# Performance work log

Hardware: AMD Instinct MI355X
Metric: run time of the kernel (lower is better)

The kernel has to match this reference:

```python
import jax, jax.numpy as jnp
import numpy as np

NUM_HEADS = 32
MAX_BIAS_LENGTH = 1024
ROPE_BASE = 10000.0


def _rope_cos_sin(seq_len, head_dim, dtype):
    half = head_dim // 2
    inv_freq = 1.0 / (ROPE_BASE ** (jnp.arange(0, half, dtype=jnp.float32) / half))
    t = jnp.arange(seq_len, dtype=jnp.float32)
    freqs = jnp.outer(t, inv_freq)  # [S, half]
    return jnp.cos(freqs).astype(dtype), jnp.sin(freqs).astype(dtype)


def _apply_rope(x, cos, sin):
    # x: [B, S, H, D]; non-interleaved (GPT-NeoX / flash-attn style) rotary
    half = x.shape[-1] // 2
    x1, x2 = x[..., :half], x[..., half:]
    c = cos[None, :, None, :]
    s = sin[None, :, None, :]
    return jnp.concatenate([x1 * c - x2 * s, x1 * s + x2 * c], axis=-1)


def setup_inputs() -> dict:
    key = jax.random.key(0)
    ks = jax.random.split(key, 7)
    B, S, Dm = 2, 2048, 2048
    std = 1.0 / np.sqrt(Dm)
    return {
        "hidden_states": jax.random.normal(ks[0], (B, S, Dm), jnp.float32),
        "Wq": jax.random.normal(ks[1], (Dm, Dm), jnp.float32) * std,
        "Wk": jax.random.normal(ks[2], (Dm, Dm), jnp.float32) * std,
        "Wv": jax.random.normal(ks[3], (Dm, Dm), jnp.float32) * std,
        "Wo": jax.random.normal(ks[4], (Dm, Dm), jnp.float32) * std,
        "learnable_bias": jax.random.normal(ks[5], (NUM_HEADS, MAX_BIAS_LENGTH), jnp.float32) * 0.001,
        "softmax_offset": jnp.zeros((NUM_HEADS,), jnp.float32),
    }


def reference(hidden_states, Wq, Wk, Wv, Wo, learnable_bias, softmax_offset):
    B, S, Dm = hidden_states.shape
    H = NUM_HEADS
    D = Dm // H
    scale = D ** -0.5

    # projections (nn.Linear: x @ W.T)
    q = (hidden_states @ Wq.T).reshape(B, S, H, D)
    k = (hidden_states @ Wk.T).reshape(B, S, H, D)
    v = (hidden_states @ Wv.T).reshape(B, S, H, D)

    cos, sin = _rope_cos_sin(S, D, q.dtype)
    q = _apply_rope(q, cos, sin)
    k = _apply_rope(k, cos, sin)

    q = q.transpose(0, 2, 1, 3)  # [B, H, S, D]
    k = k.transpose(0, 2, 1, 3)
    v = v.transpose(0, 2, 1, 3)

    scores = jnp.einsum("bhid,bhjd->bhij", q, k) * scale  # [B, H, S, S]

    # per-diagonal learnable bias: diag = i - j in [0, MAX_BIAS_LENGTH)
    i = jnp.arange(S)[:, None]
    j = jnp.arange(S)[None, :]
    diag = i - j  # [S, S]
    causal = diag >= 0
    in_band = causal & (diag < MAX_BIAS_LENGTH)
    bias = jnp.where(in_band, learnable_bias[:, jnp.clip(diag, 0, MAX_BIAS_LENGTH - 1)], 0.0)  # [H, S, S]
    scores = scores + bias[None]
    scores = jnp.where(causal[None, None], scores, -jnp.inf)

    # softmax with learnable per-head offset (attention-sink logit)
    off = softmax_offset[None, :, None]  # [1, H, 1]
    m = jnp.maximum(jnp.max(scores, axis=-1), off)  # [B, H, S]
    p = jnp.exp(scores - m[..., None])
    denom = jnp.sum(p, axis=-1) + jnp.exp(off - m)  # [B, H, S]
    out = jnp.einsum("bhij,bhjd->bhid", p, v) / denom[..., None]

    out = out.transpose(0, 2, 1, 3).reshape(B, S, Dm)
    return out @ Wo.T
```

## Files before the change

### kernel.cpp

```cpp
#include <hip/hip_runtime.h>
#include <hip/hip_bf16.h>
#include <stdint.h>

typedef __bf16 bf16x8 __attribute__((ext_vector_type(8)));
typedef float f32x4 __attribute__((ext_vector_type(4)));
typedef unsigned short u16;
typedef u16 u16x4 __attribute__((ext_vector_type(4)));

#define S_LEN 2048
#define DMODEL 2048
#define NHEADS 32
#define BATCH 2
#define MROWS (BATCH * S_LEN)
#define BIAS_LEN 1024

__device__ __forceinline__ u16 b16(float f) {
  union { __bf16 h; u16 u; } cv; cv.h = (__bf16)f; return cv.u;
}

__device__ __forceinline__ void gload16(const void* g, void* l) {
  __builtin_amdgcn_global_load_lds(
      (const __attribute__((address_space(1))) uint32_t*)g,
      (__attribute__((address_space(3))) uint32_t*)l, 16, 0, 0);
}

__global__ __launch_bounds__(256)
void cvt_bf16(const float* __restrict__ in, u16* __restrict__ out, int n) {
  int i = (blockIdx.x * 256 + threadIdx.x) * 4;
  if (i >= n) return;
  float4 v = *(const float4*)(in + i);
  u16x4 o = { b16(v.x), b16(v.y), b16(v.z), b16(v.w) };
  *(u16x4*)(out + i) = o;
}

__global__ __launch_bounds__(256)
void rope_tab(float* __restrict__ ct, float* __restrict__ st) {
  int idx = blockIdx.x * 256 + threadIdx.x;
  if (idx >= S_LEN * 32) return;
  int s = idx >> 5, d = idx & 31;
  float inv = exp2f((float)d * (-13.287712379549449f / 32.0f));
  float a = (float)s * inv;
  ct[idx] = cosf(a);
  st[idx] = sinf(a);
}

template<int EPI>
__global__ __launch_bounds__(256)
void gemm_bt(const u16* __restrict__ A, const u16* __restrict__ Bm,
             void* __restrict__ Cout,
             const float* __restrict__ ctab, const float* __restrict__ stab)
{
  __shared__ u16 sA[128 * 64];
  __shared__ u16 sB[128 * 64];
  const int tid  = threadIdx.x;
  const int lane = tid & 63;
  const int wid  = tid >> 6;
  const int wm   = wid >> 1, wn = wid & 1;
  const int lc   = lane & 15, lr = lane >> 4;
  const int tm   = blockIdx.y * 128;
  const int tn   = blockIdx.x * 128;

  f32x4 acc[4][4] = {};

  const u16* aS[4]; const u16* bS[4];
#pragma unroll
  for (int it = 0; it < 4; ++it) {
    int u = it * 256 + tid;
    int row = u >> 3;
    int ch  = (u & 7) ^ (row & 7);
    aS[it] = A  + (size_t)(tm + row) * DMODEL + ch * 8;
    bS[it] = Bm + (size_t)(tn + row) * DMODEL + ch * 8;
  }

  for (int k0 = 0; k0 < DMODEL; k0 += 64) {
    __syncthreads();
#pragma unroll
    for (int it = 0; it < 4; ++it) {
      int u = it * 256 + tid;
      gload16(aS[it] + k0, (char*)sA + u * 16);
      gload16(bS[it] + k0, (char*)sB + u * 16);
    }
    __syncthreads();
#pragma unroll
    for (int kk = 0; kk < 2; ++kk) {
      bf16x8 af[4], bq[4];
#pragma unroll
      for (int mi = 0; mi < 4; ++mi) {
        int row = wm * 64 + mi * 16 + lc;
        int ch  = (kk * 4 + lr) ^ (row & 7);
        af[mi] = *(const bf16x8*)((const char*)sA + row * 128 + ch * 16);
      }
#pragma unroll
      for (int ni = 0; ni < 4; ++ni) {
        int row = wn * 64 + ni * 16 + lc;
        int ch  = (kk * 4 + lr) ^ (row & 7);
        bq[ni] = *(const bf16x8*)((const char*)sB + row * 128 + ch * 16);
      }
#pragma unroll
      for (int mi = 0; mi < 4; ++mi)
#pragma unroll
        for (int ni = 0; ni < 4; ++ni)
          acc[mi][ni] = __builtin_amdgcn_mfma_f32_16x16x32_bf16(af[mi], bq[ni], acc[mi][ni], 0, 0, 0);
    }
  }

  if constexpr (EPI == 4) {
    float* C = (float*)Cout;
#pragma unroll
    for (int mi = 0; mi < 4; ++mi)
#pragma unroll
      for (int ni = 0; ni < 4; ++ni)
#pragma unroll
        for (int j = 0; j < 4; ++j) {
          int r = tm + wm * 64 + mi * 16 + lr * 4 + j;
          int c = tn + wn * 64 + ni * 16 + lc;
          C[(size_t)r * DMODEL + c] = acc[mi][ni][j];
        }
  } else if constexpr (EPI == 3) {
    u16* C = (u16*)Cout;
#pragma unroll
    for (int mi = 0; mi < 4; ++mi)
#pragma unroll
      for (int ni = 0; ni < 4; ++ni) {
        int col = tn + wn * 64 + ni * 16 + lc;
        int hh = col >> 6, d = col & 63;
        int m0 = tm + wm * 64 + mi * 16 + lr * 4;
        int bb = m0 >> 11, s = m0 & 2047;
        u16x4 v = { b16(acc[mi][ni][0]), b16(acc[mi][ni][1]),
                    b16(acc[mi][ni][2]), b16(acc[mi][ni][3]) };
        *(u16x4*)(C + (((size_t)bb * NHEADS + hh) * 64 + d) * S_LEN + s) = v;
      }
  } else {
    u16* C = (u16*)Cout;
#pragma unroll
    for (int mi = 0; mi < 4; ++mi)
#pragma unroll
      for (int ni = 0; ni < 2; ++ni)
#pragma unroll
        for (int j = 0; j < 4; ++j) {
          int col = tn + wn * 64 + ni * 16 + lc;
          int hh = col >> 6, dl = col & 63;
          int r = tm + wm * 64 + mi * 16 + lr * 4 + j;
          int bb = r >> 11, s = r & 2047;
          float x1 = acc[mi][ni][j], x2 = acc[mi][ni + 2][j];
          float cv = ctab[s * 32 + dl], sv = stab[s * 32 + dl];
          float o1 = x1 * cv - x2 * sv;
          float o2 = x1 * sv + x2 * cv;
          if constexpr (EPI == 1) { o1 *= 0.125f; o2 *= 0.125f; }
          size_t base = (((size_t)bb * NHEADS + hh) * S_LEN + s) * 64 + dl;
          C[base]      = b16(o1);
          C[base + 32] = b16(o2);
        }
  }
}

__global__ __launch_bounds__(512)
void attn_kernel(const u16* __restrict__ Q, const u16* __restrict__ K,
                 const u16* __restrict__ V, const float* __restrict__ biasg,
                 const float* __restrict__ offg, u16* __restrict__ O)
{
  __shared__ __align__(16) u16 sK[2][64 * 64];
  __shared__ __align__(16) u16 sV[2][64 * 64];
  __shared__ __align__(16) u16 sP[8][16 * 72];
  __shared__ float sBias[BIAS_LEN];

  const int tid = threadIdx.x, lane = tid & 63, wid = tid >> 6;
  const int lc = lane & 15, lr = lane >> 4;
  const int pi = blockIdx.x;
  const int bh = blockIdx.y;
  const int h  = bh & 31;
  const int b  = bh >> 5;
  const int qtA  = 31 - pi;
  const int myQt = (wid < 4) ? qtA : pi;
  const int qw   = myQt * 64 + (wid & 3) * 16;

  for (int i = tid; i < BIAS_LEN; i += 512) sBias[i] = biasg[h * BIAS_LEN + i];
  const float off = offg[h];

  const u16* qp = Q + ((size_t)bh * S_LEN + qw + lc) * 64;
  bf16x8 aq0 = *(const bf16x8*)(qp + lr * 8);
  bf16x8 aq1 = *(const bf16x8*)(qp + 32 + lr * 8);

  const int srow = tid >> 3;
  const int sch  = (tid & 7) ^ (srow & 7);
  const u16* kSrc = K + ((size_t)bh * S_LEN + srow) * 64 + sch * 8;
  const u16* vSrc = V + ((size_t)bh * 64 + srow) * S_LEN + sch * 8;

  float m = off, lsum = 1.0f;
  f32x4 o[4] = {};

  gload16(kSrc, (char*)sK[0] + tid * 16);
  gload16(vSrc, (char*)sV[0] + tid * 16);
  __syncthreads();

  for (int t = 0; t <= qtA; ++t) {
    const int cur = t & 1;
    if (t < qtA) {
      gload16(kSrc + (size_t)(t + 1) * 64 * 64, (char*)sK[cur ^ 1] + tid * 16);
      gload16(vSrc + (t + 1) * 64,              (char*)sV[cur ^ 1] + tid * 16);
    }

    if (t <= myQt) {
      const int kt = t * 64;
      f32x4 sc[4];
#pragma unroll
      for (int f = 0; f < 4; ++f) {
        int row = f * 16 + lc;
        bf16x8 k0 = *(const bf16x8*)((const char*)sK[cur] + row * 128 + ((lr) ^ (row & 7)) * 16);
        bf16x8 k1 = *(const bf16x8*)((const char*)sK[cur] + row * 128 + ((4 + lr) ^ (row & 7)) * 16);
        f32x4 z = {};
        z     = __builtin_amdgcn_mfma_f32_16x16x32_bf16(k0, aq0, z, 0, 0, 0);
        sc[f] = __builtin_amdgcn_mfma_f32_16x16x32_bf16(k1, aq1, z, 0, 0, 0);
      }

      const int db  = qw + lc - kt;
      const int dqt = qw - kt;
      float pvv[4][4];
      if (t == myQt) {
#pragma unroll
        for (int f = 0; f < 4; ++f)
#pragma unroll
          for (int j = 0; j < 4; ++j) {
            int dd = db - (f * 16 + lr * 4 + j);
            float bb = sBias[dd & 1023];
            pvv[f][j] = (dd >= 0) ? sc[f][j] + bb : -1e30f;
          }
      } else if (dqt <= 1008) {
#pragma unroll
        for (int f = 0; f < 4; ++f)
#pragma unroll
          for (int j = 0; j < 4; ++j)
            pvv[f][j] = sc[f][j] + sBias[db - (f * 16 + lr * 4 + j)];
      } else if (dqt < 1088) {
#pragma unroll
        for (int f = 0; f < 4; ++f)
#pragma unroll
          for (int j = 0; j < 4; ++j) {
            int dd = db - (f * 16 + lr * 4 + j);
            float bb = (dd < 1024) ? sBias[dd & 1023] : 0.0f;
            pvv[f][j] = sc[f][j] + bb;
          }
      } else {
#pragma unroll
        for (int f = 0; f < 4; ++f)
#pragma unroll
          for (int j = 0; j < 4; ++j)
            pvv[f][j] = sc[f][j];
      }

      float pmax = -1e30f;
#pragma unroll
      for (int f = 0; f < 4; ++f) {
        float a = fmaxf(fmaxf(pvv[f][0], pvv[f][1]), fmaxf(pvv[f][2], pvv[f][3]));
        pmax = fmaxf(pmax, a);
      }
      pmax = fmaxf(pmax, __shfl_xor(pmax, 16, 64));
      pmax = fmaxf(pmax, __shfl_xor(pmax, 32, 64));

      if (__any(pmax > m + 8.0f)) {
        float mn = fmaxf(m, pmax);
        float al = __expf(m - mn);
        m = mn;
        lsum *= al;
        float aj[4];
#pragma unroll
        for (int j = 0; j < 4; ++j) aj[j] = __shfl(al, lr * 4 + j, 64);
#pragma unroll
        for (int f2 = 0; f2 < 4; ++f2)
#pragma unroll
          for (int j = 0; j < 4; ++j) o[f2][j] *= aj[j];
      }

      float rsum = 0.0f;
#pragma unroll
      for (int f = 0; f < 4; ++f)
#pragma unroll
        for (int j = 0; j < 4; ++j) {
          float p = __expf(pvv[f][j] - m);
          pvv[f][j] = p;
          rsum += p;
        }
      rsum += __shfl_xor(rsum, 16, 64);
      rsum += __shfl_xor(rsum, 32, 64);
      lsum += rsum;

      u16* myP = sP[wid];
#pragma unroll
      for (int f = 0; f < 4; ++f) {
        u16x4 w = { b16(pvv[f][0]), b16(pvv[f][1]), b16(pvv[f][2]), b16(pvv[f][3]) };
        *(u16x4*)(myP + lc * 72 + f * 16 + lr * 4) = w;
      }
      __threadfence_block();

#pragma unroll
      for (int kk = 0; kk < 2; ++kk) {
        bf16x8 ap = *(const bf16x8*)(myP + lc * 72 + kk * 32 + lr * 8);
#pragma unroll
        for (int f2 = 0; f2 < 4; ++f2) {
          int drow = f2 * 16 + lc;
          int chh = (kk * 4 + lr) ^ (drow & 7);
          bf16x8 bv = *(const bf16x8*)((const char*)sV[cur] + drow * 128 + chh * 16);
          o[f2] = __builtin_amdgcn_mfma_f32_16x16x32_bf16(ap, bv, o[f2], 0, 0, 0);
        }
      }
    }
    __syncthreads();
  }

  float ls[4];
#pragma unroll
  for (int j = 0; j < 4; ++j) ls[j] = __shfl(lsum, lr * 4 + j, 64);
#pragma unroll
  for (int f2 = 0; f2 < 4; ++f2)
#pragma unroll
    for (int j = 0; j < 4; ++j) {
      int i = qw + lr * 4 + j;
      int d = f2 * 16 + lc;
      size_t addr = (((size_t)(b * S_LEN + i)) * NHEADS + h) * 64 + d;
      O[addr] = b16(o[f2][j] / ls[j]);
    }
}

extern "C" void kernel_launch(void* const* d_in, const int* in_sizes, int n_in,
                              void* d_out, int out_size, void* d_ws, size_t ws_size,
                              hipStream_t stream)
{
  const float* hs   = (const float*)d_in[0];
  const float* Wq   = (const float*)d_in[1];
  const float* Wk   = (const float*)d_in[2];
  const float* Wv   = (const float*)d_in[3];
  const float* Wo   = (const float*)d_in[4];
  const float* bias = (const float*)d_in[5];
  const float* off  = (const float*)d_in[6];

  char* p = (char*)d_ws;
  u16* hs_b = (u16*)p; p += (size_t)MROWS * DMODEL * 2;
  u16* wq_b = (u16*)p; p += (size_t)DMODEL * DMODEL * 2;
  u16* wk_b = (u16*)p; p += (size_t)DMODEL * DMODEL * 2;
  u16* wv_b = (u16*)p; p += (size_t)DMODEL * DMODEL * 2;
  u16* wo_b = (u16*)p; p += (size_t)DMODEL * DMODEL * 2;
  u16* qf   = (u16*)p; p += (size_t)MROWS * DMODEL * 2;
  u16* kf   = (u16*)p; p += (size_t)MROWS * DMODEL * 2;
  u16* vt   = (u16*)p; p += (size_t)MROWS * DMODEL * 2;
  u16* att  = (u16*)p; p += (size_t)MROWS * DMODEL * 2;
  float* ct = (float*)p; p += (size_t)S_LEN * 32 * 4;
  float* st = (float*)p; p += (size_t)S_LEN * 32 * 4;
  (void)ws_size; (void)in_sizes; (void)n_in; (void)out_size;

  cvt_bf16<<<(MROWS * DMODEL) / 1024, 256, 0, stream>>>(hs, hs_b, MROWS * DMODEL);
  cvt_bf16<<<(DMODEL * DMODEL) / 1024, 256, 0, stream>>>(Wq, wq_b, DMODEL * DMODEL);
  cvt_bf16<<<(DMODEL * DMODEL) / 1024, 256, 0, stream>>>(Wk, wk_b, DMODEL * DMODEL);
  cvt_bf16<<<(DMODEL * DMODEL) / 1024, 256, 0, stream>>>(Wv, wv_b, DMODEL * DMODEL);
  cvt_bf16<<<(DMODEL * DMODEL) / 1024, 256, 0, stream>>>(Wo, wo_b, DMODEL * DMODEL);
  rope_tab<<<(S_LEN * 32) / 256, 256, 0, stream>>>(ct, st);

  dim3 g(DMODEL / 128, MROWS / 128);
  gemm_bt<1><<<g, 256, 0, stream>>>(hs_b, wq_b, qf, ct, st);
  gemm_bt<2><<<g, 256, 0, stream>>>(hs_b, wk_b, kf, ct, st);
  gemm_bt<3><<<g, 256, 0, stream>>>(hs_b, wv_b, vt, nullptr, nullptr);
  attn_kernel<<<dim3(16, BATCH * NHEADS), 512, 0, stream>>>(qf, kf, vt, bias, off, att);
  gemm_bt<4><<<g, 256, 0, stream>>>(att, wo_b, d_out, nullptr, nullptr);
}
```

Before: 301.6 us.

## Pass P via ds_bpermute, use exp2 softmax, set MFMA priority, remap grid

The attention kernel now builds the P operand for the PV MFMA in registers using ds_bpermute, replacing the per-wave LDS staging buffer and its fence. Softmax switches to exp2, with log2(e) folded into the Q scale, the bias and the offset. MFMA sections get raised wave priority, launch bounds request 6 waves per SIMD, and the grid is flattened to a 1-D index that interleaves heads across blocks, likely for L2/XCD locality. Together these aim to cut LDS traffic, exp cost and scheduling stalls, at the risk of permute-index mistakes and register-pressure limits.

```diff
diff --git a/kernel.cpp b/kernel.cpp
--- a/kernel.cpp
+++ b/kernel.cpp
@@ -6,6 +6,7 @@
 typedef float f32x4 __attribute__((ext_vector_type(4)));
 typedef unsigned short u16;
 typedef u16 u16x4 __attribute__((ext_vector_type(4)));
+typedef uint32_t u32x4 __attribute__((ext_vector_type(4)));
 
 #define S_LEN 2048
 #define DMODEL 2048
@@ -13,6 +14,7 @@
 #define BATCH 2
 #define MROWS (BATCH * S_LEN)
 #define BIAS_LEN 1024
+#define LOG2E 1.44269504088896f
 
 __device__ __forceinline__ u16 b16(float f) {
   union { __bf16 h; u16 u; } cv; cv.h = (__bf16)f; return cv.u;
@@ -146,7 +148,9 @@
           float cv = ctab[s * 32 + dl], sv = stab[s * 32 + dl];
           float o1 = x1 * cv - x2 * sv;
           float o2 = x1 * sv + x2 * cv;
-          if constexpr (EPI == 1) { o1 *= 0.125f; o2 *= 0.125f; }
+          if constexpr (EPI == 1) {
+            o1 *= 0.125f * LOG2E; o2 *= 0.125f * LOG2E;
+          }
           size_t base = (((size_t)bb * NHEADS + hh) * S_LEN + s) * 64 + dl;
           C[base]      = b16(o1);
           C[base + 32] = b16(o2);
@@ -154,28 +158,30 @@
   }
 }
 
-__global__ __launch_bounds__(512)
+__global__ __launch_bounds__(512, 6)
 void attn_kernel(const u16* __restrict__ Q, const u16* __restrict__ K,
                  const u16* __restrict__ V, const float* __restrict__ biasg,
                  const float* __restrict__ offg, u16* __restrict__ O)
 {
   __shared__ __align__(16) u16 sK[2][64 * 64];
   __shared__ __align__(16) u16 sV[2][64 * 64];
-  __shared__ __align__(16) u16 sP[8][16 * 72];
   __shared__ float sBias[BIAS_LEN];
 
   const int tid = threadIdx.x, lane = tid & 63, wid = tid >> 6;
   const int lc = lane & 15, lr = lane >> 4;
-  const int pi = blockIdx.x;
-  const int bh = blockIdx.y;
+
+  const int L   = blockIdx.x;
+  const int idx = L >> 3;
+  const int pi  = idx >> 3;
+  const int bh  = (L & 7) + 8 * (idx & 7);
   const int h  = bh & 31;
   const int b  = bh >> 5;
   const int qtA  = 31 - pi;
   const int myQt = (wid < 4) ? qtA : pi;
   const int qw   = myQt * 64 + (wid & 3) * 16;
 
-  for (int i = tid; i < BIAS_LEN; i += 512) sBias[i] = biasg[h * BIAS_LEN + i];
-  const float off = offg[h];
+  for (int i = tid; i < BIAS_LEN; i += 512) sBias[i] = biasg[h * BIAS_LEN + i] * LOG2E;
+  const float off = offg[h] * LOG2E;
 
   const u16* qp = Q + ((size_t)bh * S_LEN + qw + lc) * 64;
   bf16x8 aq0 = *(const bf16x8*)(qp + lr * 8);
@@ -188,6 +194,10 @@
 
   float m = off, lsum = 1.0f;
   f32x4 o[4] = {};
+
+  const int idx0 = (lc + 16 * ((lr & 1) * 2)) << 2;
+  const int idx1 = idx0 + 64;
+  const bool fhi = (lr >> 1) != 0;
 
   gload16(kSrc, (char*)sK[0] + tid * 16);
   gload16(vSrc, (char*)sV[0] + tid * 16);
@@ -203,6 +213,7 @@
     if (t <= myQt) {
       const int kt = t * 64;
       f32x4 sc[4];
+      __builtin_amdgcn_s_setprio(1);
 #pragma unroll
       for (int f = 0; f < 4; ++f) {
         int row = f * 16 + lc;
@@ -212,6 +223,7 @@
         z     = __builtin_amdgcn_mfma_f32_16x16x32_bf16(k0, aq0, z, 0, 0, 0);
         sc[f] = __builtin_amdgcn_mfma_f32_16x16x32_bf16(k1, aq1, z, 0, 0, 0);
       }
+      __builtin_amdgcn_s_setprio(0);
 
       const int db  = qw + lc - kt;
       const int dqt = qw - kt;
@@ -259,7 +271,7 @@
 
       if (__any(pmax > m + 8.0f)) {
         float mn = fmaxf(m, pmax);
-        float al = __expf(m - mn);
+        float al = exp2f(m - mn);
         m = mn;
         lsum *= al;
         float aj[4];
@@ -272,29 +284,36 @@
       }
 
       float rsum = 0.0f;
-#pragma unroll
-      for (int f = 0; f < 4; ++f)
-#pragma unroll
-        for (int j = 0; j < 4; ++j) {
-          float p = __expf(pvv[f][j] - m);
-          pvv[f][j] = p;
-          rsum += p;
-        }
+      uint32_t Pp[4][2];
+#pragma unroll
+      for (int f = 0; f < 4; ++f) {
+        float p0 = exp2f(pvv[f][0] - m);
+        float p1 = exp2f(pvv[f][1] - m);
+        float p2 = exp2f(pvv[f][2] - m);
+        float p3 = exp2f(pvv[f][3] - m);
+        rsum += (p0 + p1) + (p2 + p3);
+        Pp[f][0] = (uint32_t)b16(p0) | ((uint32_t)b16(p1) << 16);
+        Pp[f][1] = (uint32_t)b16(p2) | ((uint32_t)b16(p3) << 16);
+      }
       rsum += __shfl_xor(rsum, 16, 64);
       rsum += __shfl_xor(rsum, 32, 64);
       lsum += rsum;
 
-      u16* myP = sP[wid];
-#pragma unroll
-      for (int f = 0; f < 4; ++f) {
-        u16x4 w = { b16(pvv[f][0]), b16(pvv[f][1]), b16(pvv[f][2]), b16(pvv[f][3]) };
-        *(u16x4*)(myP + lc * 72 + f * 16 + lr * 4) = w;
-      }
-      __threadfence_block();
-
 #pragma unroll
       for (int kk = 0; kk < 2; ++kk) {
-        bf16x8 ap = *(const bf16x8*)(myP + lc * 72 + kk * 32 + lr * 8);
+        uint32_t wl0 = __builtin_amdgcn_ds_bpermute(idx0, (int)Pp[2 * kk][0]);
+        uint32_t wl1 = __builtin_amdgcn_ds_bpermute(idx0, (int)Pp[2 * kk][1]);
+        uint32_t wl2 = __builtin_amdgcn_ds_bpermute(idx1, (int)Pp[2 * kk][0]);
+        uint32_t wl3 = __builtin_amdgcn_ds_bpermute(idx1, (int)Pp[2 * kk][1]);
+        uint32_t wh0 = __builtin_amdgcn_ds_bpermute(idx0, (int)Pp[2 * kk + 1][0]);
+        uint32_t wh1 = __builtin_amdgcn_ds_bpermute(idx0, (int)Pp[2 * kk + 1][1]);
+        uint32_t wh2 = __builtin_amdgcn_ds_bpermute(idx1, (int)Pp[2 * kk + 1][0]);
+        uint32_t wh3 = __builtin_amdgcn_ds_bpermute(idx1, (int)Pp[2 * kk + 1][1]);
+        u32x4 aw = { fhi ? wh0 : wl0, fhi ? wh1 : wl1,
+                     fhi ? wh2 : wl2, fhi ? wh3 : wl3 };
+        union { u32x4 u; bf16x8 bv; } cvu; cvu.u = aw;
+        bf16x8 ap = cvu.bv;
+        __builtin_amdgcn_s_setprio(1);
 #pragma unroll
         for (int f2 = 0; f2 < 4; ++f2) {
           int drow = f2 * 16 + lc;
@@ -302,6 +321,7 @@
           bf16x8 bv = *(const bf16x8*)((const char*)sV[cur] + drow * 128 + chh * 16);
           o[f2] = __builtin_amdgcn_mfma_f32_16x16x32_bf16(ap, bv, o[f2], 0, 0, 0);
         }
+        __builtin_amdgcn_s_setprio(0);
       }
     }
     __syncthreads();
@@ -358,6 +378,6 @@
   gemm_bt<1><<<g, 256, 0, stream>>>(hs_b, wq_b, qf, ct, st);
   gemm_bt<2><<<g, 256, 0, stream>>>(hs_b, wk_b, kf, ct, st);
   gemm_bt<3><<<g, 256, 0, stream>>>(hs_b, wv_b, vt, nullptr, nullptr);
-  attn_kernel<<<dim3(16, BATCH * NHEADS), 512, 0, stream>>>(qf, kf, vt, bias, off, att);
+  attn_kernel<<<dim3(16 * 64), 512, 0, stream>>>(qf, kf, vt, bias, off, att);
   gemm_bt<4><<<g, 256, 0, stream>>>(att, wo_b, d_out, nullptr, nullptr);
 }
```

Measured after the change: 312.8 us. 3.7% more time.

## Tune attention kernel: exp2 softmax, smaller P buffer, setprio, remapped grid

Applied to the files above, without the earlier changes.

Folds log2(e) into the Q scale, bias and offset so the softmax can use exp2f instead of __expf. The per-wave P staging buffer shrinks to 16x40 and is written and read in two halves with an explicit lgkmcnt wait, and the MFMA sections are wrapped in s_setprio. Launch bounds now request 6 waves per SIMD, and the 2D grid is flattened to 1D with a remapping that spreads the (batch, head) pairs across consecutive blocks. These changes target transcendental cost, LDS footprint, occupancy and scheduling, at the risk of register spills under the tighter launch bound.

```diff
diff --git a/kernel.cpp b/kernel.cpp
--- a/kernel.cpp
+++ b/kernel.cpp
@@ -13,6 +13,7 @@
 #define BATCH 2
 #define MROWS (BATCH * S_LEN)
 #define BIAS_LEN 1024
+#define LOG2E 1.44269504088896f
 
 __device__ __forceinline__ u16 b16(float f) {
   union { __bf16 h; u16 u; } cv; cv.h = (__bf16)f; return cv.u;
@@ -146,7 +147,9 @@
           float cv = ctab[s * 32 + dl], sv = stab[s * 32 + dl];
           float o1 = x1 * cv - x2 * sv;
           float o2 = x1 * sv + x2 * cv;
-          if constexpr (EPI == 1) { o1 *= 0.125f; o2 *= 0.125f; }
+          if constexpr (EPI == 1) {
+            o1 *= 0.125f * LOG2E; o2 *= 0.125f * LOG2E;
+          }
           size_t base = (((size_t)bb * NHEADS + hh) * S_LEN + s) * 64 + dl;
           C[base]      = b16(o1);
           C[base + 32] = b16(o2);
@@ -154,28 +157,31 @@
   }
 }
 
-__global__ __launch_bounds__(512)
+__global__ __launch_bounds__(512, 6)
 void attn_kernel(const u16* __restrict__ Q, const u16* __restrict__ K,
                  const u16* __restrict__ V, const float* __restrict__ biasg,
                  const float* __restrict__ offg, u16* __restrict__ O)
 {
   __shared__ __align__(16) u16 sK[2][64 * 64];
   __shared__ __align__(16) u16 sV[2][64 * 64];
-  __shared__ __align__(16) u16 sP[8][16 * 72];
+  __shared__ __align__(16) u16 sP[8][16 * 40];
   __shared__ float sBias[BIAS_LEN];
 
   const int tid = threadIdx.x, lane = tid & 63, wid = tid >> 6;
   const int lc = lane & 15, lr = lane >> 4;
-  const int pi = blockIdx.x;
-  const int bh = blockIdx.y;
+
+  const int L   = blockIdx.x;
+  const int idx = L >> 3;
+  const int pi  = idx >> 3;
+  const int bh  = (L & 7) + 8 * (idx & 7);
   const int h  = bh & 31;
   const int b  = bh >> 5;
   const int qtA  = 31 - pi;
   const int myQt = (wid < 4) ? qtA : pi;
   const int qw   = myQt * 64 + (wid & 3) * 16;
 
-  for (int i = tid; i < BIAS_LEN; i += 512) sBias[i] = biasg[h * BIAS_LEN + i];
-  const float off = offg[h];
+  for (int i = tid; i < BIAS_LEN; i += 512) sBias[i] = biasg[h * BIAS_LEN + i] * LOG2E;
+  const float off = offg[h] * LOG2E;
 
   const u16* qp = Q + ((size_t)bh * S_LEN + qw + lc) * 64;
   bf16x8 aq0 = *(const bf16x8*)(qp + lr * 8);
@@ -203,6 +209,7 @@
     if (t <= myQt) {
       const int kt = t * 64;
       f32x4 sc[4];
+      __builtin_amdgcn_s_setprio(1);
 #pragma unroll
       for (int f = 0; f < 4; ++f) {
         int row = f * 16 + lc;
@@ -212,6 +219,7 @@
         z     = __builtin_amdgcn_mfma_f32_16x16x32_bf16(k0, aq0, z, 0, 0, 0);
         sc[f] = __builtin_amdgcn_mfma_f32_16x16x32_bf16(k1, aq1, z, 0, 0, 0);
       }
+      __builtin_amdgcn_s_setprio(0);
 
       const int db  = qw + lc - kt;
       const int dqt = qw - kt;
@@ -259,7 +267,7 @@
 
       if (__any(pmax > m + 8.0f)) {
         float mn = fmaxf(m, pmax);
-        float al = __expf(m - mn);
+        float al = exp2f(m - mn);
         m = mn;
         lsum *= al;
         float aj[4];
@@ -276,7 +284,7 @@
       for (int f = 0; f < 4; ++f)
 #pragma unroll
         for (int j = 0; j < 4; ++j) {
-          float p = __expf(pvv[f][j] - m);
+          float p = exp2f(pvv[f][j] - m);
           pvv[f][j] = p;
           rsum += p;
         }
@@ -286,15 +294,17 @@
 
       u16* myP = sP[wid];
 #pragma unroll
-      for (int f = 0; f < 4; ++f) {
-        u16x4 w = { b16(pvv[f][0]), b16(pvv[f][1]), b16(pvv[f][2]), b16(pvv[f][3]) };
-        *(u16x4*)(myP + lc * 72 + f * 16 + lr * 4) = w;
-      }
-      __threadfence_block();
-
-#pragma unroll
       for (int kk = 0; kk < 2; ++kk) {
-        bf16x8 ap = *(const bf16x8*)(myP + lc * 72 + kk * 32 + lr * 8);
+#pragma unroll
+        for (int fl = 0; fl < 2; ++fl) {
+          int f = kk * 2 + fl;
+          u16x4 w = { b16(pvv[f][0]), b16(pvv[f][1]), b16(pvv[f][2]), b16(pvv[f][3]) };
+          *(u16x4*)(myP + lc * 40 + fl * 16 + lr * 4) = w;
+        }
+        asm volatile("s_waitcnt lgkmcnt(0)" ::: "memory");
+        __builtin_amdgcn_sched_barrier(0);
+        bf16x8 ap = *(const bf16x8*)(myP + lc * 40 + lr * 8);
+        __builtin_amdgcn_s_setprio(1);
 #pragma unroll
         for (int f2 = 0; f2 < 4; ++f2) {
           int drow = f2 * 16 + lc;
@@ -302,6 +312,7 @@
           bf16x8 bv = *(const bf16x8*)((const char*)sV[cur] + drow * 128 + chh * 16);
           o[f2] = __builtin_amdgcn_mfma_f32_16x16x32_bf16(ap, bv, o[f2], 0, 0, 0);
         }
+        __builtin_amdgcn_s_setprio(0);
       }
     }
     __syncthreads();
@@ -358,6 +369,6 @@
   gemm_bt<1><<<g, 256, 0, stream>>>(hs_b, wq_b, qf, ct, st);
   gemm_bt<2><<<g, 256, 0, stream>>>(hs_b, wk_b, kf, ct, st);
   gemm_bt<3><<<g, 256, 0, stream>>>(hs_b, wv_b, vt, nullptr, nullptr);
-  attn_kernel<<<dim3(16, BATCH * NHEADS), 512, 0, stream>>>(qf, kf, vt, bias, off, att);
+  attn_kernel<<<dim3(16 * 64), 512, 0, stream>>>(qf, kf, vt, bias, off, att);
   gemm_bt<4><<<g, 256, 0, stream>>>(att, wo_b, d_out, nullptr, nullptr);
 }
```

New measurement: 304.2 us. No clear change (+0.9%).
